# Kernel tuning notes

Measured on AMD Instinct MI355X. Metric: run time of the kernel, lower is better.

## Reference

```python
import jax, jax.numpy as jnp
import numpy as np

NSIDE_SEND, NSIDE_REC = 128, 64
NPIX_SEND = 12 * NSIDE_SEND * NSIDE_SEND  # 196608 edges (one per fine pixel)
NPIX_REC = 12 * NSIDE_REC * NSIDE_REC     # 49152 coarse pixels
RATIO = NPIX_SEND // NPIX_REC             # 4 children per coarse pixel
B, F_IN = 2, 128
EMBED_OUT, LIN_OUT = 64, 128
LIN_IN = EMBED_OUT + F_IN


def setup_inputs() -> dict:
    key = jax.random.key(0)
    ks = jax.random.split(key, 9)
    s = 0.02
    # buffers (deterministic, from HEALPix nested ordering)
    edge_attr = (jnp.arange(NPIX_SEND, dtype=jnp.float32) % RATIO).reshape(-1, 1)
    edge_rec = (jnp.arange(NPIX_SEND, dtype=jnp.int32) // RATIO)
    return {
        "x": jax.random.normal(ks[0], (B, NPIX_SEND, F_IN), dtype=jnp.float32),
        "edge_attr": edge_attr,
        "edge_rec": edge_rec,
        # edge embedder MLP: 1 -> 64 -> 64
        "we1": jax.random.normal(ks[1], (1, EMBED_OUT), dtype=jnp.float32) * s,
        "be1": jnp.zeros((EMBED_OUT,), dtype=jnp.float32),
        "we2": jax.random.normal(ks[2], (EMBED_OUT, EMBED_OUT), dtype=jnp.float32) * s,
        "be2": jnp.zeros((EMBED_OUT,), dtype=jnp.float32),
        # final FeedForward: 192 -> 128 -> 128
        "wf1": jax.random.normal(ks[3], (LIN_IN, LIN_OUT), dtype=jnp.float32) * s,
        "bf1": jnp.zeros((LIN_OUT,), dtype=jnp.float32),
        "wf2": jax.random.normal(ks[4], (LIN_OUT, LIN_OUT), dtype=jnp.float32) * s,
        "bf2": jnp.zeros((LIN_OUT,), dtype=jnp.float32),
    }


def reference(x, edge_attr, edge_rec, we1, be1, we2, be2, wf1, bf1, wf2, bf2):
    # edge embedding MLP over the per-edge scalar attribute  [E, embed_out]
    e = jax.nn.gelu(edge_attr @ we1 + be1) @ we2 + be2
    # broadcast over batch and concat with node features  [B, E, lin_in]
    vm = jnp.concatenate([jnp.broadcast_to(e[None], (x.shape[0],) + e.shape), x], axis=-1)
    # scatter_sum over receiver pixels along the edge axis  [B, R, lin_in]
    agg = jax.vmap(lambda v: jax.ops.segment_sum(v, edge_rec, num_segments=NPIX_REC))(vm)
    # final FeedForward
    return jax.nn.gelu(agg @ wf1 + bf1) @ wf2 + bf2
```

## Files before the change

### kernel.cpp

```cpp
#include <hip/hip_runtime.h>


#define NPIX_SEND 196608
#define NPIX_REC  49152
#define F_IN      128
#define EMB       64
#define LIN_OUT   128
#define MTOT      98304
#define BM        64
#define NBLOCKS   (MTOT / BM)

#define WS_C1 0
#define WS_W1 512
#define WS_W2 (512 + 32768)

#define LDS_H 0
#define LDS_W 16384
#define LDS_BYTES 49152

typedef __attribute__((ext_vector_type(4))) float f32x4;
typedef __attribute__((ext_vector_type(8))) short bf16x8;

__device__ __forceinline__ float gelu_tanh(float v) {
  float u = 0.7978845608028654f * (v + 0.044715f * v * v * v);
  float e = __expf(2.0f * u);
  return 0.5f * v * (1.0f + (1.0f - 2.0f / (e + 1.0f)));
}

__device__ __forceinline__ unsigned short f2bf(float f) {
  unsigned int u = __builtin_bit_cast(unsigned int, f);
  u += 0x7FFFu + ((u >> 16) & 1u);
  return (unsigned short)(u >> 16);
}

__global__ void heal_prep(const float* __restrict__ we1, const float* __restrict__ be1,
                          const float* __restrict__ we2, const float* __restrict__ be2,
                          const float* __restrict__ wf1, const float* __restrict__ bf1,
                          const float* __restrict__ wf2,
                          unsigned char* __restrict__ ws) {
  int t = threadIdx.x;
  if (blockIdx.x == 0) {
    __shared__ float G[EMB];
    __shared__ float esum[EMB];
    if (t < EMB) {
      float w = we1[t], b = be1[t];
      float g = 0.f;
      #pragma unroll
      for (int a = 0; a < 4; ++a) g += gelu_tanh((float)a * w + b);
      G[t] = g;
    }
    __syncthreads();
    if (t < EMB) {
      float s = 4.0f * be2[t];
      for (int h = 0; h < EMB; ++h) s += G[h] * we2[h * EMB + t];
      esum[t] = s;
    }
    __syncthreads();
    if (t < LIN_OUT) {
      float s = bf1[t];
      for (int i = 0; i < EMB; ++i) s += esum[i] * wf1[i * LIN_OUT + t];
      ((float*)(ws + WS_C1))[t] = s;
    }
  } else {
    int e0 = (blockIdx.x - 1) * 512 + t * 2;
    #pragma unroll
    for (int u = 0; u < 2; ++u) {
      int e = e0 + u;
      int idx = e & 16383;
      int n = idx >> 7;
      int k = idx & 127;
      float v;
      unsigned int base;
      if (e < 16384) { v = wf1[(EMB + k) * LIN_OUT + n]; base = WS_W1; }
      else           { v = wf2[k * LIN_OUT + n];         base = WS_W2; }
      unsigned int byte = (unsigned int)(n * 256 + k * 2) ^ (unsigned int)((n & 7) << 4);
      *(unsigned short*)(ws + base + byte) = f2bf(v);
    }
  }
}

__global__ __launch_bounds__(256, 3) void heal_main(
    const float* __restrict__ x, const float* __restrict__ bf2,
    const unsigned char* __restrict__ ws, float* __restrict__ out) {
  extern __shared__ unsigned char smem[];
  const int t = threadIdx.x;

  {
    const uint4* src = (const uint4*)(ws + WS_W1);
    uint4* dst = (uint4*)(smem + LDS_W);
    #pragma unroll
    for (int i = 0; i < 8; ++i) dst[t + 256 * i] = src[t + 256 * i];
  }
  uint4 w2reg[8];
  {
    const uint4* src2 = (const uint4*)(ws + WS_W2);
    #pragma unroll
    for (int i = 0; i < 8; ++i) w2reg[i] = src2[t + 256 * i];
  }

  const int gr0 = blockIdx.x * BM;
  const int b   = gr0 / NPIX_REC;
  const int rr0 = gr0 - b * NPIX_REC;
  const float* xb = x + (size_t)(b * NPIX_SEND + 4 * rr0) * F_IN;
  {
    const int kq = t & 31;
    const int mg = t >> 5;
    #pragma unroll
    for (int it = 0; it < 8; ++it) {
      int m = mg + it * 8;
      const f32x4* rp = (const f32x4*)(xb + (size_t)(4 * m) * F_IN) + kq;
      f32x4 s = rp[0] + rp[32] + rp[64] + rp[96];
      unsigned int lo = (unsigned int)f2bf(s.x) | ((unsigned int)f2bf(s.y) << 16);
      unsigned int hi = (unsigned int)f2bf(s.z) | ((unsigned int)f2bf(s.w) << 16);
      unsigned int byte = (unsigned int)(m * 256 + kq * 8) ^ (unsigned int)((m & 7) << 4);
      uint2 val; val.x = lo; val.y = hi;
      *(uint2*)(smem + LDS_H + byte) = val;
    }
  }

  const int w  = t >> 6;
  const int l  = t & 63;
  const int cr = l & 15;
  const int kg = l >> 4;
  float c1v[8], b2v[8];
  {
    const float* c1 = (const float*)(ws + WS_C1);
    #pragma unroll
    for (int f = 0; f < 8; ++f) { c1v[f] = c1[f * 16 + cr]; b2v[f] = bf2[f * 16 + cr]; }
  }

  __syncthreads();

  const int arow = w * 16 + cr;
  const unsigned int aswz = (unsigned int)((arow & 7) << 4);
  const unsigned int abase = (unsigned int)(arow * 256 + kg * 16);
  const unsigned int bswz = (unsigned int)((cr & 7) << 4);

  bf16x8 a[4];
  #pragma unroll
  for (int kk = 0; kk < 4; ++kk)
    a[kk] = *(const bf16x8*)(smem + LDS_H + ((abase + kk * 64) ^ aswz));

  f32x4 acc[8];
  #pragma unroll
  for (int f = 0; f < 8; ++f) {
    f32x4 z = {0.f, 0.f, 0.f, 0.f};
    acc[f] = z;
    unsigned int nbase = (unsigned int)((f * 16 + cr) * 256 + kg * 16);
    #pragma unroll
    for (int kk = 0; kk < 4; ++kk) {
      bf16x8 bfrag = *(const bf16x8*)(smem + LDS_W + ((nbase + kk * 64) ^ bswz));
      acc[f] = __builtin_amdgcn_mfma_f32_16x16x32_bf16(a[kk], bfrag, acc[f], 0, 0, 0);
    }
  }

  #pragma unroll
  for (int f = 0; f < 8; ++f) {
    #pragma unroll
    for (int q = 0; q < 4; ++q) {
      float v = gelu_tanh(acc[f][q] + c1v[f]);
      int hrow = w * 16 + kg * 4 + q;
      unsigned int byte = (unsigned int)(hrow * 256 + (f * 16 + cr) * 2)
                        ^ (unsigned int)((hrow & 7) << 4);
      *(unsigned short*)(smem + LDS_H + byte) = f2bf(v);
    }
  }

  __syncthreads();

  bf16x8 a2[4];
  #pragma unroll
  for (int kk = 0; kk < 4; ++kk)
    a2[kk] = *(const bf16x8*)(smem + LDS_H + ((abase + kk * 64) ^ aswz));

  {
    uint4* dst = (uint4*)(smem + LDS_W);
    #pragma unroll
    for (int i = 0; i < 8; ++i) dst[t + 256 * i] = w2reg[i];
  }
  __syncthreads();

  f32x4 acc2[8];
  #pragma unroll
  for (int f = 0; f < 8; ++f) {
    f32x4 z = {0.f, 0.f, 0.f, 0.f};
    acc2[f] = z;
    unsigned int nbase = (unsigned int)((f * 16 + cr) * 256 + kg * 16);
    #pragma unroll
    for (int kk = 0; kk < 4; ++kk) {
      bf16x8 bfrag = *(const bf16x8*)(smem + LDS_W + ((nbase + kk * 64) ^ bswz));
      acc2[f] = __builtin_amdgcn_mfma_f32_16x16x32_bf16(a2[kk], bfrag, acc2[f], 0, 0, 0);
    }
  }

  #pragma unroll
  for (int q = 0; q < 4; ++q) {
    int orow = gr0 + w * 16 + kg * 4 + q;
    float* op = out + (size_t)orow * LIN_OUT;
    #pragma unroll
    for (int f = 0; f < 8; ++f)
      op[f * 16 + cr] = acc2[f][q] + b2v[f];
  }
}

extern "C" void kernel_launch(void* const* d_in, const int* in_sizes, int n_in,
                              void* d_out, int out_size, void* d_ws, size_t ws_size,
                              hipStream_t stream) {
  const float* x   = (const float*)d_in[0];
  const float* we1 = (const float*)d_in[3];
  const float* be1 = (const float*)d_in[4];
  const float* we2 = (const float*)d_in[5];
  const float* be2 = (const float*)d_in[6];
  const float* wf1 = (const float*)d_in[7];
  const float* bf1 = (const float*)d_in[8];
  const float* wf2 = (const float*)d_in[9];
  const float* bf2 = (const float*)d_in[10];
  float* out = (float*)d_out;
  unsigned char* ws = (unsigned char*)d_ws;

  hipLaunchKernelGGL(heal_prep, dim3(65), dim3(256), 0, stream,
                     we1, be1, we2, be2, wf1, bf1, wf2, ws);
  hipLaunchKernelGGL(heal_main, dim3(NBLOCKS), dim3(256), LDS_BYTES, stream,
                     x, bf2, ws, out);
}
```

Before: 70.45 us.

## Fold child-pixel summation into K-extended MFMA and drop LDS staging of x

Each thread now loads its own x rows straight from global memory and converts them to bf16 A fragments. The four-child segment sum is folded into the first GEMM by running 16 MFMAs over K=512 that reuse the same weight fragments, instead of summing in fp32 and staging through LDS. This removes the LDS round-trip and one barrier, but quadruples the first-GEMM MFMA work and register pressure (16 A fragments). The W2 global load is moved later, and the bf16 rounding now happens per child before summation.

```diff
diff --git a/kernel.cpp b/kernel.cpp
--- a/kernel.cpp
+++ b/kernel.cpp
@@ -27,10 +27,19 @@
   return 0.5f * v * (1.0f + (1.0f - 2.0f / (e + 1.0f)));
 }
 
-__device__ __forceinline__ unsigned short f2bf(float f) {
+__device__ __forceinline__ unsigned int f2bf(float f) {
   unsigned int u = __builtin_bit_cast(unsigned int, f);
   u += 0x7FFFu + ((u >> 16) & 1u);
-  return (unsigned short)(u >> 16);
+  return u >> 16;
+}
+
+__device__ __forceinline__ bf16x8 pack8(f32x4 u, f32x4 v) {
+  union { bf16x8 h; unsigned int w[4]; } o;
+  o.w[0] = f2bf(u.x) | (f2bf(u.y) << 16);
+  o.w[1] = f2bf(u.z) | (f2bf(u.w) << 16);
+  o.w[2] = f2bf(v.x) | (f2bf(v.y) << 16);
+  o.w[3] = f2bf(v.z) | (f2bf(v.w) << 16);
+  return o.h;
 }
 
 __global__ void heal_prep(const float* __restrict__ we1, const float* __restrict__ be1,
@@ -74,7 +83,7 @@
       if (e < 16384) { v = wf1[(EMB + k) * LIN_OUT + n]; base = WS_W1; }
       else           { v = wf2[k * LIN_OUT + n];         base = WS_W2; }
       unsigned int byte = (unsigned int)(n * 256 + k * 2) ^ (unsigned int)((n & 7) << 4);
-      *(unsigned short*)(ws + base + byte) = f2bf(v);
+      *(unsigned short*)(ws + base + byte) = f2bf(v) | 0u ? (unsigned short)f2bf(v) : (unsigned short)0;
     }
   }
 }
@@ -84,6 +93,11 @@
     const unsigned char* __restrict__ ws, float* __restrict__ out) {
   extern __shared__ unsigned char smem[];
   const int t = threadIdx.x;
+  const int w = t >> 6, l = t & 63;
+  const int cr = l & 15, kg = l >> 4;
+
+  const int gr0 = blockIdx.x * BM;
+  const float* xb = x + (size_t)gr0 * 512;
 
   {
     const uint4* src = (const uint4*)(ws + WS_W1);
@@ -91,37 +105,30 @@
     #pragma unroll
     for (int i = 0; i < 8; ++i) dst[t + 256 * i] = src[t + 256 * i];
   }
-  uint4 w2reg[8];
-  {
-    const uint4* src2 = (const uint4*)(ws + WS_W2);
-    #pragma unroll
-    for (int i = 0; i < 8; ++i) w2reg[i] = src2[t + 256 * i];
-  }
-
-  const int gr0 = blockIdx.x * BM;
-  const int b   = gr0 / NPIX_REC;
-  const int rr0 = gr0 - b * NPIX_REC;
-  const float* xb = x + (size_t)(b * NPIX_SEND + 4 * rr0) * F_IN;
-  {
-    const int kq = t & 31;
-    const int mg = t >> 5;
-    #pragma unroll
-    for (int it = 0; it < 8; ++it) {
-      int m = mg + it * 8;
-      const f32x4* rp = (const f32x4*)(xb + (size_t)(4 * m) * F_IN) + kq;
-      f32x4 s = rp[0] + rp[32] + rp[64] + rp[96];
-      unsigned int lo = (unsigned int)f2bf(s.x) | ((unsigned int)f2bf(s.y) << 16);
-      unsigned int hi = (unsigned int)f2bf(s.z) | ((unsigned int)f2bf(s.w) << 16);
-      unsigned int byte = (unsigned int)(m * 256 + kq * 8) ^ (unsigned int)((m & 7) << 4);
-      uint2 val; val.x = lo; val.y = hi;
-      *(uint2*)(smem + LDS_H + byte) = val;
-    }
-  }
-
-  const int w  = t >> 6;
-  const int l  = t & 63;
-  const int cr = l & 15;
-  const int kg = l >> 4;
+
+  const int arow = w * 16 + cr;
+  bf16x8 a[16];
+  {
+    f32x4 xA[4][2], xB[4][2];
+    const float* rowb = xb + (size_t)(4 * arow) * F_IN + kg * 8;
+    #define ISSUE(BUF, G)                                                   \
+      _Pragma("unroll")                                                     \
+      for (int i = 0; i < 4; ++i) {                                         \
+        int kc = (G) * 4 + i;                                               \
+        const f32x4* p = (const f32x4*)(rowb + (kc >> 2) * 128 + (kc & 3) * 32); \
+        BUF[i][0] = p[0]; BUF[i][1] = p[1];                                 \
+      }
+    #define CONV(BUF, G)                                                    \
+      _Pragma("unroll")                                                     \
+      for (int i = 0; i < 4; ++i) a[(G) * 4 + i] = pack8(BUF[i][0], BUF[i][1]);
+    ISSUE(xA, 0); ISSUE(xB, 1);
+    CONV(xA, 0);  ISSUE(xA, 2);
+    CONV(xB, 1);  ISSUE(xB, 3);
+    CONV(xA, 2);  CONV(xB, 3);
+    #undef ISSUE
+    #undef CONV
+  }
+
   float c1v[8], b2v[8];
   {
     const float* c1 = (const float*)(ws + WS_C1);
@@ -131,15 +138,9 @@
 
   __syncthreads();
 
-  const int arow = w * 16 + cr;
   const unsigned int aswz = (unsigned int)((arow & 7) << 4);
   const unsigned int abase = (unsigned int)(arow * 256 + kg * 16);
   const unsigned int bswz = (unsigned int)((cr & 7) << 4);
-
-  bf16x8 a[4];
-  #pragma unroll
-  for (int kk = 0; kk < 4; ++kk)
-    a[kk] = *(const bf16x8*)(smem + LDS_H + ((abase + kk * 64) ^ aswz));
 
   f32x4 acc[8];
   #pragma unroll
@@ -147,11 +148,13 @@
     f32x4 z = {0.f, 0.f, 0.f, 0.f};
     acc[f] = z;
     unsigned int nbase = (unsigned int)((f * 16 + cr) * 256 + kg * 16);
-    #pragma unroll
-    for (int kk = 0; kk < 4; ++kk) {
-      bf16x8 bfrag = *(const bf16x8*)(smem + LDS_W + ((nbase + kk * 64) ^ bswz));
-      acc[f] = __builtin_amdgcn_mfma_f32_16x16x32_bf16(a[kk], bfrag, acc[f], 0, 0, 0);
-    }
+    bf16x8 b4[4];
+    #pragma unroll
+    for (int i = 0; i < 4; ++i)
+      b4[i] = *(const bf16x8*)(smem + LDS_W + ((nbase + i * 64) ^ bswz));
+    #pragma unroll
+    for (int kc = 0; kc < 16; ++kc)
+      acc[f] = __builtin_amdgcn_mfma_f32_16x16x32_bf16(a[kc], b4[kc & 3], acc[f], 0, 0, 0);
   }
 
   #pragma unroll
@@ -162,16 +165,23 @@
       int hrow = w * 16 + kg * 4 + q;
       unsigned int byte = (unsigned int)(hrow * 256 + (f * 16 + cr) * 2)
                         ^ (unsigned int)((hrow & 7) << 4);
-      *(unsigned short*)(smem + LDS_H + byte) = f2bf(v);
-    }
-  }
-
-  __syncthreads();
+      *(unsigned short*)(smem + LDS_H + byte) = (unsigned short)f2bf(v);
+    }
+  }
 
   bf16x8 a2[4];
   #pragma unroll
   for (int kk = 0; kk < 4; ++kk)
     a2[kk] = *(const bf16x8*)(smem + LDS_H + ((abase + kk * 64) ^ aswz));
+
+  uint4 w2reg[8];
+  {
+    const uint4* src2 = (const uint4*)(ws + WS_W2);
+    #pragma unroll
+    for (int i = 0; i < 8; ++i) w2reg[i] = src2[t + 256 * i];
+  }
+
+  __syncthreads();
 
   {
     uint4* dst = (uint4*)(smem + LDS_W);
```

Measured after the change: 72.82 us. 1.03x slower.

## Fuse weight prep into main kernel, recompute constants and bf16 weights per block

Applied to the files above, without the earlier changes.

Removes the separate prep kernel and its workspace by having every block read the fp32 weights directly, convert them to swizzled bf16 in LDS, and recompute the edge-embedding constant vector with small per-block loops. This drops one kernel launch and the dependency between launches. In exchange, every block repeats redundant weight loads, bf16 conversion and the serial 64-step embedding chain. It also adds raw barriers and more register pressure from holding the converted weights.

```diff
diff --git a/kernel.cpp b/kernel.cpp
--- a/kernel.cpp
+++ b/kernel.cpp
@@ -1,22 +1,18 @@
 #include <hip/hip_runtime.h>
 
 
-#define NPIX_SEND 196608
 #define NPIX_REC  49152
 #define F_IN      128
-#define EMB       64
-#define LIN_OUT   128
 #define MTOT      98304
 #define BM        64
 #define NBLOCKS   (MTOT / BM)
 
-#define WS_C1 0
-#define WS_W1 512
-#define WS_W2 (512 + 32768)
-
-#define LDS_H 0
-#define LDS_W 16384
-#define LDS_BYTES 49152
+#define LDS_C 0
+#define LDS_G 512
+#define LDS_E 768
+#define LDS_X 1024
+#define LDS_W 17408
+#define LDS_TOT 50176
 
 typedef __attribute__((ext_vector_type(4))) float f32x4;
 typedef __attribute__((ext_vector_type(8))) short bf16x8;
@@ -27,106 +23,128 @@
   return 0.5f * v * (1.0f + (1.0f - 2.0f / (e + 1.0f)));
 }
 
-__device__ __forceinline__ unsigned short f2bf(float f) {
+__device__ __forceinline__ unsigned int f2bf(float f) {
   unsigned int u = __builtin_bit_cast(unsigned int, f);
   u += 0x7FFFu + ((u >> 16) & 1u);
-  return (unsigned short)(u >> 16);
-}
-
-__global__ void heal_prep(const float* __restrict__ we1, const float* __restrict__ be1,
-                          const float* __restrict__ we2, const float* __restrict__ be2,
-                          const float* __restrict__ wf1, const float* __restrict__ bf1,
-                          const float* __restrict__ wf2,
-                          unsigned char* __restrict__ ws) {
-  int t = threadIdx.x;
-  if (blockIdx.x == 0) {
-    __shared__ float G[EMB];
-    __shared__ float esum[EMB];
-    if (t < EMB) {
-      float w = we1[t], b = be1[t];
-      float g = 0.f;
-      #pragma unroll
-      for (int a = 0; a < 4; ++a) g += gelu_tanh((float)a * w + b);
-      G[t] = g;
-    }
-    __syncthreads();
-    if (t < EMB) {
-      float s = 4.0f * be2[t];
-      for (int h = 0; h < EMB; ++h) s += G[h] * we2[h * EMB + t];
-      esum[t] = s;
-    }
-    __syncthreads();
-    if (t < LIN_OUT) {
-      float s = bf1[t];
-      for (int i = 0; i < EMB; ++i) s += esum[i] * wf1[i * LIN_OUT + t];
-      ((float*)(ws + WS_C1))[t] = s;
-    }
-  } else {
-    int e0 = (blockIdx.x - 1) * 512 + t * 2;
-    #pragma unroll
-    for (int u = 0; u < 2; ++u) {
-      int e = e0 + u;
-      int idx = e & 16383;
-      int n = idx >> 7;
-      int k = idx & 127;
-      float v;
-      unsigned int base;
-      if (e < 16384) { v = wf1[(EMB + k) * LIN_OUT + n]; base = WS_W1; }
-      else           { v = wf2[k * LIN_OUT + n];         base = WS_W2; }
-      unsigned int byte = (unsigned int)(n * 256 + k * 2) ^ (unsigned int)((n & 7) << 4);
-      *(unsigned short*)(ws + base + byte) = f2bf(v);
-    }
-  }
-}
-
-__global__ __launch_bounds__(256, 3) void heal_main(
-    const float* __restrict__ x, const float* __restrict__ bf2,
-    const unsigned char* __restrict__ ws, float* __restrict__ out) {
-  extern __shared__ unsigned char smem[];
+  return u >> 16;
+}
+
+__device__ __forceinline__ void rawbar() {
+  asm volatile("s_waitcnt lgkmcnt(0)" ::: "memory");
+  __builtin_amdgcn_s_barrier();
+  __builtin_amdgcn_sched_barrier(0);
+}
+
+__global__ __launch_bounds__(256, 3) void heal_all(
+    const float* __restrict__ x,
+    const float* __restrict__ we1, const float* __restrict__ be1,
+    const float* __restrict__ we2, const float* __restrict__ be2,
+    const float* __restrict__ wf1, const float* __restrict__ bf1,
+    const float* __restrict__ wf2, const float* __restrict__ bf2,
+    float* __restrict__ out) {
+  __shared__ unsigned char smem[LDS_TOT];
   const int t = threadIdx.x;
+  const int w = t >> 6, l = t & 63;
+  const int cr = l & 15, kg = l >> 4;
+
+  const int gr0 = blockIdx.x * BM;
+  const float* xb = x + (size_t)gr0 * 512;
+
+  const int pk = t >> 4, pn = t & 15;
+  f32x4 w1v[8][2];
+  #pragma unroll
+  for (int rr = 0; rr < 8; ++rr) {
+    const f32x4* p = (const f32x4*)(wf1 + (size_t)(64 + pk * 8 + rr) * 128 + pn * 8);
+    w1v[rr][0] = p[0]; w1v[rr][1] = p[1];
+  }
+
+  float b2v[8];
+  #pragma unroll
+  for (int f = 0; f < 8; ++f) b2v[f] = bf2[f * 16 + cr];
 
   {
-    const uint4* src = (const uint4*)(ws + WS_W1);
-    uint4* dst = (uint4*)(smem + LDS_W);
-    #pragma unroll
-    for (int i = 0; i < 8; ++i) dst[t + 256 * i] = src[t + 256 * i];
-  }
-  uint4 w2reg[8];
+    const int kq = l & 31;
+    const int rh = l >> 5;
+    #pragma unroll 4
+    for (int it = 0; it < 8; ++it) {
+      int m = w * 16 + it * 2 + rh;
+      const f32x4* rp = (const f32x4*)(xb + (size_t)(4 * m) * F_IN) + kq;
+      f32x4 s = (rp[0] + rp[32]) + (rp[64] + rp[96]);
+      uint2 val;
+      val.x = f2bf(s.x) | (f2bf(s.y) << 16);
+      val.y = f2bf(s.z) | (f2bf(s.w) << 16);
+      unsigned int byte = (unsigned int)(m * 256 + kq * 8) ^ (unsigned int)((m & 7) << 4);
+      *(uint2*)(smem + LDS_X + byte) = val;
+    }
+  }
+
+  if (t < 64) {
+    float wv = we1[t], bv = be1[t];
+    float g = 0.f;
+    #pragma unroll
+    for (int a = 0; a < 4; ++a) g += gelu_tanh((float)a * wv + bv);
+    ((float*)(smem + LDS_G))[t] = g;
+  }
+  rawbar();
+  if (t < 64) {
+    float s = 4.0f * be2[t];
+    const float* G = (const float*)(smem + LDS_G);
+    #pragma unroll 8
+    for (int h = 0; h < 64; ++h) s += G[h] * we2[h * 64 + t];
+    ((float*)(smem + LDS_E))[t] = s;
+  }
+  rawbar();
+  if (t < 128) {
+    float s = bf1[t];
+    const float* E = (const float*)(smem + LDS_E);
+    #pragma unroll 8
+    for (int i = 0; i < 64; ++i) s += E[i] * wf1[(size_t)i * 128 + t];
+    ((float*)(smem + LDS_C))[t] = s;
+  }
+
+  #pragma unroll
+  for (int j = 0; j < 8; ++j) {
+    float e0 = (j < 4) ? w1v[0][0][j] : w1v[0][1][j - 4];
+    float e1 = (j < 4) ? w1v[1][0][j] : w1v[1][1][j - 4];
+    float e2 = (j < 4) ? w1v[2][0][j] : w1v[2][1][j - 4];
+    float e3 = (j < 4) ? w1v[3][0][j] : w1v[3][1][j - 4];
+    float e4 = (j < 4) ? w1v[4][0][j] : w1v[4][1][j - 4];
+    float e5 = (j < 4) ? w1v[5][0][j] : w1v[5][1][j - 4];
+    float e6 = (j < 4) ? w1v[6][0][j] : w1v[6][1][j - 4];
+    float e7 = (j < 4) ? w1v[7][0][j] : w1v[7][1][j - 4];
+    uint4 o;
+    o.x = f2bf(e0) | (f2bf(e1) << 16);
+    o.y = f2bf(e2) | (f2bf(e3) << 16);
+    o.z = f2bf(e4) | (f2bf(e5) << 16);
+    o.w = f2bf(e6) | (f2bf(e7) << 16);
+    int n = pn * 8 + j;
+    unsigned int byte = (unsigned int)(n * 256) + (unsigned int)((pk ^ j) << 4);
+    *(uint4*)(smem + LDS_W + byte) = o;
+  }
+
+  uint4 o2[8];
   {
-    const uint4* src2 = (const uint4*)(ws + WS_W2);
-    #pragma unroll
-    for (int i = 0; i < 8; ++i) w2reg[i] = src2[t + 256 * i];
-  }
-
-  const int gr0 = blockIdx.x * BM;
-  const int b   = gr0 / NPIX_REC;
-  const int rr0 = gr0 - b * NPIX_REC;
-  const float* xb = x + (size_t)(b * NPIX_SEND + 4 * rr0) * F_IN;
-  {
-    const int kq = t & 31;
-    const int mg = t >> 5;
-    #pragma unroll
-    for (int it = 0; it < 8; ++it) {
-      int m = mg + it * 8;
-      const f32x4* rp = (const f32x4*)(xb + (size_t)(4 * m) * F_IN) + kq;
-      f32x4 s = rp[0] + rp[32] + rp[64] + rp[96];
-      unsigned int lo = (unsigned int)f2bf(s.x) | ((unsigned int)f2bf(s.y) << 16);
-      unsigned int hi = (unsigned int)f2bf(s.z) | ((unsigned int)f2bf(s.w) << 16);
-      unsigned int byte = (unsigned int)(m * 256 + kq * 8) ^ (unsigned int)((m & 7) << 4);
-      uint2 val; val.x = lo; val.y = hi;
-      *(uint2*)(smem + LDS_H + byte) = val;
-    }
-  }
-
-  const int w  = t >> 6;
-  const int l  = t & 63;
-  const int cr = l & 15;
-  const int kg = l >> 4;
-  float c1v[8], b2v[8];
-  {
-    const float* c1 = (const float*)(ws + WS_C1);
-    #pragma unroll
-    for (int f = 0; f < 8; ++f) { c1v[f] = c1[f * 16 + cr]; b2v[f] = bf2[f * 16 + cr]; }
+    f32x4 w2v[8][2];
+    #pragma unroll
+    for (int rr = 0; rr < 8; ++rr) {
+      const f32x4* p = (const f32x4*)(wf2 + (size_t)(pk * 8 + rr) * 128 + pn * 8);
+      w2v[rr][0] = p[0]; w2v[rr][1] = p[1];
+    }
+    #pragma unroll
+    for (int j = 0; j < 8; ++j) {
+      float e0 = (j < 4) ? w2v[0][0][j] : w2v[0][1][j - 4];
+      float e1 = (j < 4) ? w2v[1][0][j] : w2v[1][1][j - 4];
+      float e2 = (j < 4) ? w2v[2][0][j] : w2v[2][1][j - 4];
+      float e3 = (j < 4) ? w2v[3][0][j] : w2v[3][1][j - 4];
+      float e4 = (j < 4) ? w2v[4][0][j] : w2v[4][1][j - 4];
+      float e5 = (j < 4) ? w2v[5][0][j] : w2v[5][1][j - 4];
+      float e6 = (j < 4) ? w2v[6][0][j] : w2v[6][1][j - 4];
+      float e7 = (j < 4) ? w2v[7][0][j] : w2v[7][1][j - 4];
+      o2[j].x = f2bf(e0) | (f2bf(e1) << 16);
+      o2[j].y = f2bf(e2) | (f2bf(e3) << 16);
+      o2[j].z = f2bf(e4) | (f2bf(e5) << 16);
+      o2[j].w = f2bf(e6) | (f2bf(e7) << 16);
+    }
   }
 
   __syncthreads();
@@ -139,7 +157,14 @@
   bf16x8 a[4];
   #pragma unroll
   for (int kk = 0; kk < 4; ++kk)
-    a[kk] = *(const bf16x8*)(smem + LDS_H + ((abase + kk * 64) ^ aswz));
+    a[kk] = *(const bf16x8*)(smem + LDS_X + ((abase + kk * 64) ^ aswz));
+
+  float c1v[8];
+  {
+    const float* c1 = (const float*)(smem + LDS_C);
+    #pragma unroll
+    for (int f = 0; f < 8; ++f) c1v[f] = c1[f * 16 + cr];
+  }
 
   f32x4 acc[8];
   #pragma unroll
@@ -162,7 +187,7 @@
       int hrow = w * 16 + kg * 4 + q;
       unsigned int byte = (unsigned int)(hrow * 256 + (f * 16 + cr) * 2)
                         ^ (unsigned int)((hrow & 7) << 4);
-      *(unsigned short*)(smem + LDS_H + byte) = f2bf(v);
+      *(unsigned short*)(smem + LDS_X + byte) = (unsigned short)f2bf(v);
     }
   }
 
@@ -171,12 +196,13 @@
   bf16x8 a2[4];
   #pragma unroll
   for (int kk = 0; kk < 4; ++kk)
-    a2[kk] = *(const bf16x8*)(smem + LDS_H + ((abase + kk * 64) ^ aswz));
-
-  {
-    uint4* dst = (uint4*)(smem + LDS_W);
-    #pragma unroll
-    for (int i = 0; i < 8; ++i) dst[t + 256 * i] = w2reg[i];
+    a2[kk] = *(const bf16x8*)(smem + LDS_X + ((abase + kk * 64) ^ aswz));
+
+  #pragma unroll
+  for (int j = 0; j < 8; ++j) {
+    int n = pn * 8 + j;
+    unsigned int byte = (unsigned int)(n * 256) + (unsigned int)((pk ^ j) << 4);
+    *(uint4*)(smem + LDS_W + byte) = o2[j];
   }
   __syncthreads();
 
@@ -196,7 +222,7 @@
   #pragma unroll
   for (int q = 0; q < 4; ++q) {
     int orow = gr0 + w * 16 + kg * 4 + q;
-    float* op = out + (size_t)orow * LIN_OUT;
+    float* op = out + (size_t)orow * 128;
     #pragma unroll
     for (int f = 0; f < 8; ++f)
       op[f * 16 + cr] = acc2[f][q] + b2v[f];
@@ -216,10 +242,7 @@
   const float* wf2 = (const float*)d_in[9];
   const float* bf2 = (const float*)d_in[10];
   float* out = (float*)d_out;
-  unsigned char* ws = (unsigned char*)d_ws;
-
-  hipLaunchKernelGGL(heal_prep, dim3(65), dim3(256), 0, stream,
-                     we1, be1, we2, be2, wf1, bf1, wf2, ws);
-  hipLaunchKernelGGL(heal_main, dim3(NBLOCKS), dim3(256), LDS_BYTES, stream,
-                     x, bf2, ws, out);
-}
+
+  hipLaunchKernelGGL(heal_all, dim3(NBLOCKS), dim3(256), 0, stream,
+                     x, we1, be1, we2, be2, wf1, bf1, wf2, bf2, out);
+}
```

After: 71.09 us. Within noise of the previous version (+0.9%).
